# Kernel optimization log

Measured on AMD Instinct MI355X. Metric: run time of the kernel, lower is better.

Reference implementation:

```python
import jax, jax.numpy as jnp
import numpy as np

B, S, D, I, C = 4, 512, 512, 1024, 64
BASE_LR = 0.01
EPS = 1e-6


def _rms(x, w):
    return x * jax.lax.rsqrt(jnp.mean(x * x, axis=-1, keepdims=True) + EPS) * w


def _mem_apply(p, x):
    # 2-layer MLP memory: x + RMSNorm(W1 @ silu(W0 @ x))
    h = jax.nn.silu(x @ p["w0"].T)
    y = h @ p["w1"].T
    return x + _rms(y, p["ln"])


def _mem_loss(p, inp, tgt, w):
    # ((target - pred)^2 * theta).mean(-1).sum() over batch; w is scalar theta_t
    pred = _mem_apply(p, inp)
    return jnp.sum(jnp.mean((tgt - pred) ** 2 * w, axis=-1))


def _neural_memory(x, wq, wk, wv, q_norm_w, k_norm_w, alpha_w, alpha_b,
                   theta_w, theta_b, eta_w, eta_b, m_w0, m_w1, m_ln):
    b, s, d = x.shape
    nC = s // C
    params0 = {"w0": m_w0, "w1": m_w1, "ln": m_ln}
    surpr0 = jax.tree_util.tree_map(jnp.zeros_like, params0)
    xs = x.reshape(b, nC, C, d).transpose(1, 0, 2, 3)  # [nC, B, C, D]

    # per-token grads: vmap over sequence dim 1, shared params (in_dims=None)
    grad_fn = jax.vmap(jax.grad(_mem_loss), in_axes=(None, 1, 1, 0))
    idx = jnp.arange(C)

    def step(carry, xc):
        params, surpr = carry
        # adaptive gates: Linear -> sum over batch -> sigmoid (shapes [C])
        al = jax.nn.sigmoid(jnp.sum(xc @ alpha_w.T + alpha_b, axis=0))[:, 0]
        th = jax.nn.sigmoid(jnp.sum(xc @ theta_w.T + theta_b, axis=0))[:, 0] * BASE_LR
        et = jax.nn.sigmoid(jnp.sum(xc @ eta_w.T + eta_b, axis=0))[:, 0]
        k = _rms(jax.nn.silu(xc @ wk.T), k_norm_w)  # [B, C, D]
        v = jax.nn.silu(xc @ wv.T)
        grads = grad_fn(params, k, v, th)  # each leaf [C, *param_shape]
        # eta decay matrix E[m,n] = prod_{i=n+1}^m eta_i for n<=m, else 0
        M0 = jnp.where(idx[:, None] > idx[None, :], et[:, None], 1.0)
        Emat = jnp.where(idx[None, :] <= idx[:, None], jnp.cumprod(M0, axis=0), 0.0)
        c_eta = jnp.cumprod(et)  # prod_{0..m} eta
        beta = 1.0 - al
        bc_last = jnp.cumprod(beta)[-1]
        bt = jnp.cumprod(beta[::-1])[::-1]  # bt[m] = prod_{m..C-1} beta
        w_beta = jnp.concatenate([bt[1:], jnp.ones((1,), et.dtype)])

        def upd(pS, pM, u):
            # S_t = eta_t * S_{t-1} - u_t ; M_t = beta_t * M_{t-1} + S_t (vectorized)
            ex = (slice(None),) + (None,) * pS.ndim
            S_all = c_eta[ex] * pS - jnp.einsum("mn,n...->m...", Emat, u)
            newM = pM * bc_last + jnp.einsum("m,m...->...", w_beta, S_all)
            return newM, S_all[-1]

        res = {n: upd(surpr[n], params[n], grads[n]) for n in params}
        new_params = {n: res[n][0] for n in params}
        new_surpr = {n: res[n][1] for n in params}
        return (new_params, new_surpr), None

    (paramsF, _surprF), _ = jax.lax.scan(step, (params0, surpr0), xs)
    # retrieve from updated memory
    q = _rms(jax.nn.silu(x @ wq.T), q_norm_w)
    return _mem_apply(paramsF, q)


def setup_inputs() -> dict:
    key = jax.random.key(0)
    ks = jax.random.split(key, 12)

    def xavier(k, shape):
        lim = float(np.sqrt(6.0 / (shape[0] + shape[1])))
        return jax.random.uniform(k, shape, jnp.float32, -lim, lim)

    return {
        "x": jax.random.normal(ks[0], (B, S, D), jnp.float32),
        "wq": xavier(ks[1], (D, D)),
        "wk": xavier(ks[2], (D, D)),
        "wv": xavier(ks[3], (D, D)),
        "q_norm_w": jnp.ones((D,), jnp.float32),
        "k_norm_w": jnp.ones((D,), jnp.float32),
        "alpha_w": xavier(ks[4], (1, D)),
        "alpha_b": jnp.zeros((1,), jnp.float32),
        "theta_w": xavier(ks[5], (1, D)),
        "theta_b": jnp.zeros((1,), jnp.float32),
        "eta_w": xavier(ks[6], (1, D)),
        "eta_b": jnp.zeros((1,), jnp.float32),
        "m_w0": xavier(ks[7], (I, D)),
        "m_w1": xavier(ks[8], (D, I)),
        "m_ln": jnp.ones((D,), jnp.float32),
    }


def reference(x, wq, wk, wv, q_norm_w, k_norm_w, alpha_w, alpha_b,
              theta_w, theta_b, eta_w, eta_b, m_w0, m_w1, m_ln):
    return _neural_memory(x, wq, wk, wv, q_norm_w, k_norm_w, alpha_w, alpha_b,
                          theta_w, theta_b, eta_w, eta_b, m_w0, m_w1, m_ln)
```

## Files before the change

kernel.cpp:

```cpp
#include <hip/hip_runtime.h>
#include <math.h>

#define EPS 1e-6f

namespace {

typedef unsigned short u16;
typedef unsigned int u32;
typedef __bf16 bf16x8 __attribute__((ext_vector_type(8)));
typedef float f32x4 __attribute__((ext_vector_type(4)));
typedef u16 u16x8 __attribute__((ext_vector_type(8)));

constexpr int Bb = 4, Ss = 512, Dd = 512, Ii = 1024, Cc = 64;
constexpr int nCk = 8, RowsC = 256, RowsAll = 2048;

__device__ __forceinline__ float sigmoidf_(float x) { return 1.f / (1.f + expf(-x)); }
__device__ __forceinline__ float siluf_(float x)    { return x / (1.f + expf(-x)); }

__device__ __forceinline__ u16 f2bf(float f) {
  u32 u = __float_as_uint(f);
  u32 r = u + 0x7fffu + ((u >> 16) & 1u);
  return (u16)(r >> 16);
}
__device__ __forceinline__ float bf2f(u16 u) {
  return __uint_as_float(((u32)u) << 16);
}

__device__ __forceinline__ void llds16(const u16* g, u16* l) {
  __builtin_amdgcn_global_load_lds((__attribute__((address_space(1))) void*)g,
                                   (__attribute__((address_space(3))) void*)l,
                                   16, 0, 0);
}

__device__ __forceinline__ void drain_barrier() {
  asm volatile("s_waitcnt vmcnt(0)" ::: "memory");
  __builtin_amdgcn_s_barrier();
}

__device__ __forceinline__ float wave_sum(float v) {
  #pragma unroll
  for (int m = 32; m > 0; m >>= 1) v += __shfl_xor(v, m, 64);
  return v;
}

__device__ __forceinline__ float block_reduce_sum(float v, float* red) {
  int tid = threadIdx.x;
  red[tid] = v; __syncthreads();
  for (int s = 128; s > 0; s >>= 1) {
    if (tid < s) red[tid] += red[tid + s];
    __syncthreads();
  }
  float r = red[0]; __syncthreads();
  return r;
}

struct WS {
  float *w0c, *Sw0, *w1c, *Sw1, *lnc, *Sln, *tmpK, *Krows, *Vrows,
        *Yp, *gyr, *alv, *thv, *etv, *wBv, *wEv, *scal, *Qb, *Yr;
  u16 *xcb, *wkvqb, *w0b, *w1b, *w1tb, *Kb, *KT, *Ht, *dZb,
      *dYb, *dYtW, *dYtE, *dHtW, *dHtE, *Qbb, *Hrb;
};
__host__ __device__ inline WS mkws(char* base) {
  WS s; char* p = base + 256;
#define CF(nm, n) s.nm = (float*)p; p += (size_t)(n) * 4;
#define CU(nm, n) s.nm = (u16*)p;   p += (size_t)(n) * 2;
  CF(w0c, Ii*Dd) CF(Sw0, Ii*Dd) CF(w1c, Dd*Ii) CF(Sw1, Dd*Ii)
  CF(lnc, Dd) CF(Sln, Dd)
  CF(tmpK, (size_t)RowsAll*Dd) CF(Krows, (size_t)RowsAll*Dd) CF(Vrows, (size_t)RowsAll*Dd)
  CF(Yp, (size_t)16*RowsC*Dd) CF(gyr, RowsC*Dd)
  CF(alv, Ss) CF(thv, Ss) CF(etv, Ss) CF(wBv, nCk*RowsC) CF(wEv, nCk*RowsC) CF(scal, nCk*4)
  CF(Qb, (size_t)RowsAll*Dd) CF(Yr, (size_t)RowsAll*Dd)
  CU(xcb, (size_t)RowsAll*Dd) CU(wkvqb, (size_t)3*Dd*Dd)
  CU(w0b, (size_t)Ii*Dd) CU(w1b, (size_t)2*Dd*Ii) CU(w1tb, (size_t)2*Ii*Dd)
  CU(Kb, (size_t)RowsAll*Dd) CU(KT, (size_t)RowsAll*Dd)
  CU(Ht, RowsC*Ii) CU(dZb, RowsC*Ii)
  CU(dYb, RowsC*Dd) CU(dYtW, RowsC*Dd) CU(dYtE, RowsC*Dd)
  CU(dHtW, RowsC*Ii) CU(dHtE, RowsC*Ii)
  CU(Qbb, (size_t)RowsAll*Dd) CU(Hrb, (size_t)RowsAll*Ii)
#undef CF
#undef CU
  return s;
}

template<int BK, int NBUF, int EPI>
__device__ void tile64(
    u16* smA, u16* smB,
    const u16* __restrict__ A, const u16* __restrict__ Bt,
    int K, int N, int bm, int bn,
    float* C0, float* C1, float* C2,
    u16* CbT, u16* CbT2,
    const u16* Zb, const float* wB, const float* wE, int trM)
{
  constexpr int CPR = BK / 8;
  constexpr int NISS = (64 * CPR) / 256;
  constexpr int BUF = 64 * BK;
  const int tid = threadIdx.x;
  const int l = tid & 63, lr = l & 15, lq = l >> 4;
  const int w = tid >> 6, wr = w >> 1, wc = w & 1;

  f32x4 acc[2][2];
  #pragma unroll
  for (int i = 0; i < 2; ++i)
    #pragma unroll
    for (int j = 0; j < 2; ++j) acc[i][j] = f32x4{0.f, 0.f, 0.f, 0.f};

  auto stage = [&](int k0, int buf) {
    u16* dA = smA + buf * BUF;
    u16* dB = smB + buf * BUF;
    #pragma unroll
    for (int i = 0; i < NISS; ++i) {
      int e = i * 256 + tid;
      int r = e / CPR, c = (e & (CPR - 1)) ^ (r & (CPR - 1));
      llds16(A  + (size_t)(bm + r) * K + k0 + c * 8, dA + e * 8);
      llds16(Bt + (size_t)(bn + r) * K + k0 + c * 8, dB + e * 8);
    }
  };

  stage(0, 0);
  drain_barrier();
  const int nt = K / BK;
  int cur = 0;
  for (int t = 0; t < nt; ++t) {
    if (t + 1 < nt) stage((t + 1) * BK, (cur ^ 1) & (NBUF - 1));
    const u16* sA = smA + cur * BUF;
    const u16* sB = smB + cur * BUF;
    #pragma unroll
    for (int kk = 0; kk < BK / 32; ++kk) {
      bf16x8 av[2], bv[2];
      #pragma unroll
      for (int m = 0; m < 2; ++m) {
        int r = wr * 32 + m * 16 + lr;
        int c = (kk * 4 + lq) ^ (r & (CPR - 1));
        av[m] = *reinterpret_cast<const bf16x8*>(&sA[r * BK + c * 8]);
      }
      #pragma unroll
      for (int n = 0; n < 2; ++n) {
        int r = wc * 32 + n * 16 + lr;
        int c = (kk * 4 + lq) ^ (r & (CPR - 1));
        bv[n] = *reinterpret_cast<const bf16x8*>(&sB[r * BK + c * 8]);
      }
      #pragma unroll
      for (int m = 0; m < 2; ++m)
        #pragma unroll
        for (int n = 0; n < 2; ++n)
          acc[m][n] = __builtin_amdgcn_mfma_f32_16x16x32_bf16(av[m], bv[n], acc[m][n], 0, 0, 0);
    }
    drain_barrier();
    cur = (cur ^ 1) & (NBUF - 1);
  }

  #pragma unroll
  for (int m = 0; m < 2; ++m) {
    int gr0 = bm + wr * 32 + m * 16 + lq * 4;
    float wbq[4], weq[4];
    if (EPI == 3) {
      #pragma unroll
      for (int q = 0; q < 4; ++q) { wbq[q] = wB[gr0 + q]; weq[q] = wE[gr0 + q]; }
    }
    #pragma unroll
    for (int n = 0; n < 2; ++n) {
      int gc = bn + wc * 32 + n * 16 + lr;
      ushort4 t1, t2;
      #pragma unroll
      for (int q = 0; q < 4; ++q) {
        float v = acc[m][n][q];
        size_t idx = (size_t)(gr0 + q) * N + gc;
        if (EPI == 0) {
          C0[idx] = v;
        } else if (EPI == 1) {
          size_t rb = (size_t)(gr0 + q) * Dd;
          if (gc < Dd)            C0[rb + gc] = v;
          else if (gc < 2 * Dd)   C1[rb + gc - Dd] = siluf_(v);
          else                    C2[rb + gc - 2 * Dd] = v;
        } else if (EPI == 3) {
          float dh = v * bf2f(Zb[idx]);
          ((u16*)&t1)[q] = f2bf(dh * wbq[q]);
          ((u16*)&t2)[q] = f2bf(dh * weq[q]);
        }
      }
      if (EPI == 3) {
        *reinterpret_cast<ushort4*>(&CbT[(size_t)gc * trM + gr0]) = t1;
        *reinterpret_cast<ushort4*>(&CbT2[(size_t)gc * trM + gr0]) = t2;
      }
    }
  }
}

template<int BK, int NBUF, bool TR>
__device__ void gtile64(
    u16* smA, u16* smB, u16* smE,
    const u16* __restrict__ AW, const u16* __restrict__ AE,
    const u16* __restrict__ Bt,
    float* P, float* Sm, u16* Pb, u16* PbT, const float* scal,
    int M, int N, int K, int bm, int bn)
{
  constexpr int CPR = BK / 8;
  constexpr int NISS = (64 * CPR) / 256;
  constexpr int BUF = 64 * BK;
  const int tid = threadIdx.x;
  const int l = tid & 63, lr = l & 15, lq = l >> 4;
  const int w = tid >> 6, wr = w >> 1, wc = w & 1;

  f32x4 aM[2][2], aE[2][2];
  #pragma unroll
  for (int i = 0; i < 2; ++i)
    #pragma unroll
    for (int j = 0; j < 2; ++j) {
      aM[i][j] = f32x4{0.f, 0.f, 0.f, 0.f};
      aE[i][j] = f32x4{0.f, 0.f, 0.f, 0.f};
    }

  auto stage = [&](int k0, int buf) {
    u16* dA = smA + buf * BUF;
    u16* dE = smE + buf * BUF;
    u16* dB = smB + buf * BUF;
    #pragma unroll
    for (int i = 0; i < NISS; ++i) {
      int e = i * 256 + tid;
      int r = e / CPR, c = (e & (CPR - 1)) ^ (r & (CPR - 1));
      llds16(AW + (size_t)(bm + r) * K + k0 + c * 8, dA + e * 8);
      llds16(AE + (size_t)(bm + r) * K + k0 + c * 8, dE + e * 8);
      llds16(Bt + (size_t)(bn + r) * K + k0 + c * 8, dB + e * 8);
    }
  };

  stage(0, 0);
  drain_barrier();
  const int nt = K / BK;
  int cur = 0;
  for (int t = 0; t < nt; ++t) {
    if (t + 1 < nt) stage((t + 1) * BK, (cur ^ 1) & (NBUF - 1));
    const u16* sA = smA + cur * BUF;
    const u16* sE = smE + cur * BUF;
    const u16* sB = smB + cur * BUF;
    #pragma unroll
    for (int kk = 0; kk < BK / 32; ++kk) {
      bf16x8 awv[2], aev[2], bv[2];
      #pragma unroll
      for (int m = 0; m < 2; ++m) {
        int r = wr * 32 + m * 16 + lr;
        int c = (kk * 4 + lq) ^ (r & (CPR - 1));
        awv[m] = *reinterpret_cast<const bf16x8*>(&sA[r * BK + c * 8]);
        aev[m] = *reinterpret_cast<const bf16x8*>(&sE[r * BK + c * 8]);
      }
      #pragma unroll
      for (int n = 0; n < 2; ++n) {
        int r = wc * 32 + n * 16 + lr;
        int c = (kk * 4 + lq) ^ (r & (CPR - 1));
        bv[n] = *reinterpret_cast<const bf16x8*>(&sB[r * BK + c * 8]);
      }
      #pragma unroll
      for (int m = 0; m < 2; ++m)
        #pragma unroll
        for (int n = 0; n < 2; ++n) {
          aM[m][n] = __builtin_amdgcn_mfma_f32_16x16x32_bf16(awv[m], bv[n], aM[m][n], 0, 0, 0);
          aE[m][n] = __builtin_amdgcn_mfma_f32_16x16x32_bf16(aev[m], bv[n], aE[m][n], 0, 0, 0);
        }
    }
    drain_barrier();
    cur = (cur ^ 1) & (NBUF - 1);
  }

  float s0 = scal[0], s1 = scal[1], s2 = scal[2];
  #pragma unroll
  for (int m = 0; m < 2; ++m) {
    int gr0 = bm + wr * 32 + m * 16 + lq * 4;
    #pragma unroll
    for (int n = 0; n < 2; ++n) {
      int gc = bn + wc * 32 + n * 16 + lr;
      ushort4 t1;
      #pragma unroll
      for (int q = 0; q < 4; ++q) {
        size_t idx = (size_t)(gr0 + q) * N + gc;
        float p = P[idx], s = Sm[idx];
        float np = s0 * p + s1 * s - aM[m][n][q];
        float ns = s2 * s - aE[m][n][q];
        P[idx] = np; Sm[idx] = ns;
        Pb[idx] = f2bf(np);
        if (TR) ((u16*)&t1)[q] = f2bf(np);
      }
      if (TR) *reinterpret_cast<ushort4*>(&PbT[(size_t)gc * M + gr0]) = t1;
    }
  }
}


__global__ __launch_bounds__(256) void z0y_k(
    const u16* __restrict__ Kbc, const u16* __restrict__ w0b,
    const u16* __restrict__ w1b,
    u16* __restrict__ Ht, u16* __restrict__ dZb, float* __restrict__ Yp)
{
  __shared__ __align__(16) u16 sm[4 * 64 * 128 + 64 * 64];
  u16* Hs = sm + 4 * 64 * 128;
  const int tid = threadIdx.x;
  const int l = tid & 63, lr = l & 15, lq = l >> 4;
  const int w = tid >> 6, wr = w >> 1, wc = w & 1;
  const int tj = blockIdx.x, tr = blockIdx.y;
  const int bm = tr * 64, bn = tj * 64;

  {
    constexpr int BK = 128, CPR = 16, NISS = 4, BUF = 64 * BK;
    u16* smA = sm; u16* smB = sm + 2 * BUF;
    f32x4 acc[2][2];
    #pragma unroll
    for (int i = 0; i < 2; ++i)
      #pragma unroll
      for (int j = 0; j < 2; ++j) acc[i][j] = f32x4{0.f, 0.f, 0.f, 0.f};

    auto stage = [&](int k0, int buf) {
      u16* dA = smA + buf * BUF;
      u16* dB = smB + buf * BUF;
      #pragma unroll
      for (int i = 0; i < NISS; ++i) {
        int e = i * 256 + tid;
        int r = e / CPR, c = (e & (CPR - 1)) ^ (r & (CPR - 1));
        llds16(Kbc + (size_t)(bm + r) * Dd + k0 + c * 8, dA + e * 8);
        llds16(w0b + (size_t)(bn + r) * Dd + k0 + c * 8, dB + e * 8);
      }
    };
    stage(0, 0);
    drain_barrier();
    int cur = 0;
    for (int t = 0; t < 4; ++t) {
      if (t + 1 < 4) stage((t + 1) * BK, cur ^ 1);
      const u16* sA = smA + cur * BUF;
      const u16* sB = smB + cur * BUF;
      #pragma unroll
      for (int kk = 0; kk < 4; ++kk) {
        bf16x8 av[2], bv[2];
        #pragma unroll
        for (int m = 0; m < 2; ++m) {
          int r = wr * 32 + m * 16 + lr;
          int c = (kk * 4 + lq) ^ (r & (CPR - 1));
          av[m] = *reinterpret_cast<const bf16x8*>(&sA[r * BK + c * 8]);
        }
        #pragma unroll
        for (int n = 0; n < 2; ++n) {
          int r = wc * 32 + n * 16 + lr;
          int c = (kk * 4 + lq) ^ (r & (CPR - 1));
          bv[n] = *reinterpret_cast<const bf16x8*>(&sB[r * BK + c * 8]);
        }
        #pragma unroll
        for (int m = 0; m < 2; ++m)
          #pragma unroll
          for (int n = 0; n < 2; ++n)
            acc[m][n] = __builtin_amdgcn_mfma_f32_16x16x32_bf16(av[m], bv[n], acc[m][n], 0, 0, 0);
      }
      drain_barrier();
      cur ^= 1;
    }

    #pragma unroll
    for (int i = 0; i < 16; ++i) {
      int e = i * 256 + tid;
      int r = e >> 3, c = (e & 7) ^ (r & 7);
      llds16(w1b + (size_t)r * Ii + bn + c * 8, sm + e * 8);
    }

    #pragma unroll
    for (int m = 0; m < 2; ++m) {
      int gr0 = bm + wr * 32 + m * 16 + lq * 4;
      int rl0 = wr * 32 + m * 16 + lq * 4;
      #pragma unroll
      for (int n = 0; n < 2; ++n) {
        int gc = bn + wc * 32 + n * 16 + lr;
        int cl = wc * 32 + n * 16 + lr;
        ushort4 t1;
        #pragma unroll
        for (int q = 0; q < 4; ++q) {
          float v = acc[m][n][q];
          float sg = 1.f / (1.f + expf(-v));
          float h = v * sg;
          float ds = sg * (1.f + v * (1.f - sg));
          u16 hb = f2bf(h);
          ((u16*)&t1)[q] = hb;
          dZb[(size_t)(gr0 + q) * Ii + gc] = f2bf(ds);
          int rl = rl0 + q;
          Hs[rl * 64 + ((((cl >> 3) ^ (rl & 7)) << 3) | (cl & 7))] = hb;
        }
        *reinterpret_cast<ushort4*>(&Ht[(size_t)gc * RowsC + gr0]) = t1;
      }
    }
  }

  asm volatile("s_waitcnt vmcnt(0)" ::: "memory");
  __syncthreads();

  {
    f32x4 yacc[2][16];
    #pragma unroll
    for (int m = 0; m < 2; ++m)
      #pragma unroll
      for (int n = 0; n < 16; ++n) yacc[m][n] = f32x4{0.f, 0.f, 0.f, 0.f};

    #pragma unroll
    for (int kk = 0; kk < 2; ++kk) {
      bf16x8 av[2];
      #pragma unroll
      for (int m = 0; m < 2; ++m) {
        int r = wr * 32 + m * 16 + lr;
        int c = (kk * 4 + lq) ^ (r & 7);
        av[m] = *reinterpret_cast<const bf16x8*>(&Hs[r * 64 + c * 8]);
      }
      #pragma unroll
      for (int n = 0; n < 16; ++n) {
        int r = wc * 256 + n * 16 + lr;
        int c = (kk * 4 + lq) ^ (r & 7);
        bf16x8 bv = *reinterpret_cast<const bf16x8*>(&sm[r * 64 + c * 8]);
        #pragma unroll
        for (int m = 0; m < 2; ++m)
          yacc[m][n] = __builtin_amdgcn_mfma_f32_16x16x32_bf16(av[m], bv, yacc[m][n], 0, 0, 0);
      }
    }

    float* Yo = Yp + (size_t)tj * RowsC * Dd;
    #pragma unroll
    for (int m = 0; m < 2; ++m) {
      int gr0 = bm + wr * 32 + m * 16 + lq * 4;
      #pragma unroll
      for (int n = 0; n < 16; ++n) {
        int gc = wc * 256 + n * 16 + lr;
        #pragma unroll
        for (int q = 0; q < 4; ++q)
          Yo[(size_t)(gr0 + q) * Dd + gc] = yacc[m][n][q];
      }
    }
  }
}

__global__ __launch_bounds__(256) void s4_k(
    const u16* __restrict__ dYb, const u16* __restrict__ w1t_cur,
    const u16* __restrict__ dZb, u16* dHtW, u16* dHtE,
    const float* __restrict__ gyr, float* lnc, float* Sln,
    const u16* __restrict__ dYtW, const u16* __restrict__ dYtE,
    const u16* __restrict__ Ht,
    float* w1c, float* Sw1, u16* w1b_new, u16* w1t_new,
    const float* wB, const float* wE, const float* scal)
{
  __shared__ __align__(16) u16 sm[6 * 64 * 128];
  int j = blockIdx.x;
  if (j < 64) {
    int tm = j & 3, tn = j >> 2;
    tile64<128, 2, 3>(sm, sm + 2 * 64 * 128, dYb, w1t_cur, Dd, Ii,
                      tm * 64, tn * 64,
                      nullptr, nullptr, nullptr, dHtW, dHtE,
                      dZb, wB, wE, RowsC);
  } else if (j < 66) {
    int d = (j - 64) * 256 + threadIdx.x;
    float sm2 = 0.f, se2 = 0.f;
    for (int r = 0; r < RowsC; ++r) {
      float vv = gyr[(size_t)r * Dd + d];
      sm2 += wB[r] * vv; se2 += wE[r] * vv;
    }
    float pp = lnc[d], sn = Sln[d];
    lnc[d] = scal[0] * pp + scal[1] * sn - sm2;
    Sln[d] = scal[2] * sn - se2;
  } else {
    int q = j - 66;
    gtile64<128, 2, true>(sm, sm + 2 * 64 * 128, sm + 4 * 64 * 128,
                          dYtW, dYtE, Ht, w1c, Sw1, w1b_new, w1t_new,
                          scal, Dd, Ii, RowsC, (q >> 4) * 64, (q & 15) * 64);
  }
}

__global__ __launch_bounds__(256) void g2b_k(
    const u16* __restrict__ dHtW, const u16* __restrict__ dHtE,
    const u16* __restrict__ KTc,
    float* w0c, float* Sw0, u16* w0b, const float* scal)
{
  __shared__ __align__(16) u16 sm[6 * 64 * 128];
  int j = blockIdx.x;
  gtile64<128, 2, false>(sm, sm + 2 * 64 * 128, sm + 4 * 64 * 128,
                         dHtW, dHtE, KTc, w0c, Sw0, w0b, nullptr,
                         scal, Ii, Dd, RowsC, (j >> 3) * 64, (j & 7) * 64);
}

__global__ __launch_bounds__(256) void kvq_k(
    const u16* __restrict__ xcb, const u16* __restrict__ wkvqb,
    float* tmpK, float* Vrows, float* Yq, char* ws)
{
  __shared__ __align__(16) u16 sm[4 * 64 * 128];
  int j = blockIdx.x;
  if (j < 768) {
    int tn = j % 24, tm = j / 24;
    tile64<128, 2, 1>(sm, sm + 2 * 64 * 128, xcb, wkvqb, Dd, 3 * Dd,
                      tm * 64, tn * 64,
                      tmpK, Vrows, Yq, nullptr, nullptr,
                      nullptr, nullptr, nullptr, 0);
    return;
  }
  if (threadIdx.x != 0) return;
  WS S = mkws(ws);
  int ci = j - 768;
  const float* alc = S.alv + ci * Cc;
  const float* etc_ = S.etv + ci * Cc;
  float beta[Cc], wb[Cc], ce[Cc], E[Cc], T[Cc];
  for (int i = 0; i < Cc; ++i) beta[i] = 1.f - alc[i];
  wb[Cc - 1] = 1.f;
  for (int m = Cc - 2; m >= 0; --m) wb[m] = wb[m + 1] * beta[m + 1];
  float bc_last = wb[0] * beta[0];
  float p = 1.f, A = 0.f;
  for (int m = 0; m < Cc; ++m) { p *= etc_[m]; ce[m] = p; A += wb[m] * ce[m]; }
  E[Cc - 1] = 1.f; T[Cc - 1] = 1.f;
  for (int n = Cc - 2; n >= 0; --n) {
    E[n] = E[n + 1] * etc_[n + 1];
    T[n] = wb[n] + etc_[n + 1] * T[n + 1];
  }
  for (int b = 0; b < Bb; ++b)
    for (int t = 0; t < Cc; ++t) {
      S.wBv[ci * RowsC + b * Cc + t] = T[t];
      S.wEv[ci * RowsC + b * Cc + t] = E[t];
    }
  S.scal[ci * 4 + 0] = bc_last; S.scal[ci * 4 + 1] = A; S.scal[ci * 4 + 2] = ce[Cc - 1];
}

template<int EPI>
__global__ __launch_bounds__(256) void mgemm128_k(
    const u16* __restrict__ A, const u16* __restrict__ Bt,
    float* C0, u16* Cb, int M, int N, int K)
{
  constexpr int TS = 128, BK = 64;
  constexpr int BUF = TS * BK;
  __shared__ __align__(16) u16 As[2 * BUF];
  __shared__ __align__(16) u16 Bs[2 * BUF];
  const int tid = threadIdx.x;
  const int l = tid & 63, lr = l & 15, lq = l >> 4;
  const int w = tid >> 6, wr = w >> 1, wc = w & 1;
  const int bm = blockIdx.y * TS, bn = blockIdx.x * TS;

  f32x4 acc[4][4];
  #pragma unroll
  for (int i = 0; i < 4; ++i)
    #pragma unroll
    for (int j = 0; j < 4; ++j) acc[i][j] = f32x4{0.f, 0.f, 0.f, 0.f};

  auto stage = [&](int k0, int buf) {
    u16* dA = As + buf * BUF;
    u16* dB = Bs + buf * BUF;
    #pragma unroll
    for (int i = 0; i < 4; ++i) {
      int e = i * 256 + tid;
      int r = e >> 3, c = (e & 7) ^ (r & 7);
      llds16(A  + (size_t)(bm + r) * K + k0 + c * 8, dA + e * 8);
      llds16(Bt + (size_t)(bn + r) * K + k0 + c * 8, dB + e * 8);
    }
  };

  stage(0, 0);
  drain_barrier();
  const int nt = K / BK;
  int cur = 0;
  for (int t = 0; t < nt; ++t) {
    if (t + 1 < nt) stage((t + 1) * BK, cur ^ 1);
    const u16* sA = As + cur * BUF;
    const u16* sB = Bs + cur * BUF;
    #pragma unroll
    for (int kk = 0; kk < 2; ++kk) {
      bf16x8 av[4], bv[4];
      #pragma unroll
      for (int m = 0; m < 4; ++m) {
        int r = wr * 64 + m * 16 + lr;
        int c = (kk * 4 + lq) ^ (r & 7);
        av[m] = *reinterpret_cast<const bf16x8*>(&sA[r * BK + c * 8]);
      }
      #pragma unroll
      for (int n = 0; n < 4; ++n) {
        int r = wc * 64 + n * 16 + lr;
        int c = (kk * 4 + lq) ^ (r & 7);
        bv[n] = *reinterpret_cast<const bf16x8*>(&sB[r * BK + c * 8]);
      }
      #pragma unroll
      for (int m = 0; m < 4; ++m)
        #pragma unroll
        for (int n = 0; n < 4; ++n)
          acc[m][n] = __builtin_amdgcn_mfma_f32_16x16x32_bf16(av[m], bv[n], acc[m][n], 0, 0, 0);
    }
    drain_barrier();
    cur ^= 1;
  }

  #pragma unroll
  for (int m = 0; m < 4; ++m) {
    int gr0 = bm + wr * 64 + m * 16 + lq * 4;
    #pragma unroll
    for (int n = 0; n < 4; ++n) {
      int gc = bn + wc * 64 + n * 16 + lr;
      #pragma unroll
      for (int q = 0; q < 4; ++q) {
        size_t idx = (size_t)(gr0 + q) * N + gc;
        float v = acc[m][n][q];
        if (EPI == 0) C0[idx] = v;
        else          Cb[idx] = f2bf(siluf_(v));
      }
    }
  }
}

__global__ __launch_bounds__(256) void init_k(
    const float* __restrict__ x,
    const float* __restrict__ aw, const float* __restrict__ ab,
    const float* __restrict__ tw, const float* __restrict__ tb,
    const float* __restrict__ ew, const float* __restrict__ eb,
    const float* __restrict__ wq, const float* __restrict__ wkw,
    const float* __restrict__ wvw, const float* __restrict__ mw0,
    const float* __restrict__ mw1, const float* __restrict__ mln,
    char* ws)
{
  WS S = mkws(ws);
  const int tid = threadIdx.x;
  if (blockIdx.x < 512) {
    __shared__ float red[256];
    int s = blockIdx.x;
    int ci = s >> 6, t = s & 63;
    float sa = 0.f, st = 0.f, se = 0.f;
    for (int b = 0; b < Bb; ++b) {
      const float* xr = x + ((size_t)b * Ss + s) * Dd;
      u16* dst = S.xcb + ((size_t)(ci * RowsC + b * Cc + t)) * Dd;
      for (int d = tid; d < Dd; d += 256) {
        float v = xr[d];
        dst[d] = f2bf(v);
        sa += v * aw[d]; st += v * tw[d]; se += v * ew[d];
      }
    }
    sa = block_reduce_sum(sa, red);
    st = block_reduce_sum(st, red);
    se = block_reduce_sum(se, red);
    if (tid == 0) {
      S.alv[s] = sigmoidf_(sa + Bb * ab[0]);
      S.thv[s] = sigmoidf_(st + Bb * tb[0]) * 0.01f;
      S.etv[s] = sigmoidf_(se + Bb * eb[0]);
    }
    return;
  }
  if (blockIdx.x < 640) {
    __shared__ float t[64][65];
    int tt = blockIdx.x - 512;
    int br = (tt & 7) * 64, bc = (tt >> 3) * 64;
    #pragma unroll
    for (int i = 0; i < 16; ++i) {
      int e = tid + i * 256;
      int r = e >> 6, c = e & 63;
      t[r][c] = mw1[(size_t)(br + r) * Ii + bc + c];
    }
    __syncthreads();
    #pragma unroll
    for (int i = 0; i < 16; ++i) {
      int e = tid + i * 256;
      int rr = e >> 6, cc = e & 63;
      S.w1tb[(size_t)(bc + rr) * Dd + br + cc] = f2bf(t[cc][rr]);
    }
    return;
  }
  const int i0 = (blockIdx.x - 640) * 256 + tid;
  const int stride = 512 * 256;
  for (int i = i0; i < (Dd * Dd) / 4; i += stride) {
    float4 v = ((const float4*)wkw)[i];
    ushort4 o; o.x = f2bf(v.x); o.y = f2bf(v.y); o.z = f2bf(v.z); o.w = f2bf(v.w);
    ((ushort4*)S.wkvqb)[i] = o;
    v = ((const float4*)wvw)[i];
    o.x = f2bf(v.x); o.y = f2bf(v.y); o.z = f2bf(v.z); o.w = f2bf(v.w);
    ((ushort4*)S.wkvqb)[i + (Dd * Dd) / 4] = o;
    v = ((const float4*)wq)[i];
    o.x = f2bf(v.x); o.y = f2bf(v.y); o.z = f2bf(v.z); o.w = f2bf(v.w);
    ((ushort4*)S.wkvqb)[i + (Dd * Dd) / 2] = o;
  }
  for (int i = i0; i < (Ii * Dd) / 4; i += stride) {
    float4 z4; z4.x = z4.y = z4.z = z4.w = 0.f;
    float4 v = ((const float4*)mw0)[i];
    ((float4*)S.w0c)[i] = v; ((float4*)S.Sw0)[i] = z4;
    ushort4 o; o.x = f2bf(v.x); o.y = f2bf(v.y); o.z = f2bf(v.z); o.w = f2bf(v.w);
    ((ushort4*)S.w0b)[i] = o;
    v = ((const float4*)mw1)[i];
    ((float4*)S.w1c)[i] = v; ((float4*)S.Sw1)[i] = z4;
    o.x = f2bf(v.x); o.y = f2bf(v.y); o.z = f2bf(v.z); o.w = f2bf(v.w);
    ((ushort4*)S.w1b)[i] = o;
  }
  for (int i = i0; i < Dd; i += stride) { S.lnc[i] = mln[i]; S.Sln[i] = 0.f; }
}

__global__ __launch_bounds__(256) void norm2_k(
    const float* __restrict__ tmpK, const float* __restrict__ Yq,
    float* Krows, u16* Kb, u16* KT,
    float* Qb, u16* Qbb,
    const float* __restrict__ kn, const float* __restrict__ qn)
{
  __shared__ u16 lt[4][Dd];
  const int tid = threadIdx.x, w = tid >> 6, l = tid & 63;
  const bool isQ = blockIdx.x >= 512;
  const int r0 = (isQ ? (int)blockIdx.x - 512 : (int)blockIdx.x) * 4;
  const int row = r0 + w, d0 = l * 8;
  const float* in = (isQ ? Yq : tmpK) + (size_t)row * Dd + d0;
  const float* nw = (isQ ? qn : kn) + d0;
  float v[8];
  *(float4*)&v[0] = *(const float4*)in;
  *(float4*)&v[4] = *(const float4*)(in + 4);
  float ss = 0.f;
  #pragma unroll
  for (int j = 0; j < 8; ++j) { v[j] = siluf_(v[j]); ss += v[j] * v[j]; }
  ss = wave_sum(ss);
  float rr = rsqrtf(ss / (float)Dd + EPS);
  float nv[8];
  *(float4*)&nv[0] = *(const float4*)nw;
  *(float4*)&nv[4] = *(const float4*)(nw + 4);
  float y[8]; u16x8 pb;
  #pragma unroll
  for (int j = 0; j < 8; ++j) { y[j] = v[j] * rr * nv[j]; pb[j] = f2bf(y[j]); }
  float* outf = (isQ ? Qb : Krows) + (size_t)row * Dd + d0;
  u16* outb = (isQ ? Qbb : Kb) + (size_t)row * Dd + d0;
  *(float4*)outf       = *(float4*)&y[0];
  *(float4*)(outf + 4) = *(float4*)&y[4];
  *(u16x8*)outb = pb;
  if (!isQ) {
    int ci = r0 >> 8, rloc = r0 & 255;
    u16* KTc = KT + (size_t)ci * Dd * RowsC;
    #pragma unroll
    for (int j = 0; j < 8; ++j) lt[w][d0 + j] = pb[j];
    __syncthreads();
    for (int d = tid; d < Dd; d += 256) {
      ushort4 pk;
      pk.x = lt[0][d]; pk.y = lt[1][d]; pk.z = lt[2][d]; pk.w = lt[3][d];
      *reinterpret_cast<ushort4*>(&KTc[(size_t)d * RowsC + rloc]) = pk;
    }
  }
}

__global__ __launch_bounds__(256) void loss_back4_k(
    const float* __restrict__ Kr, const float* __restrict__ Vr,
    const float* __restrict__ Yp, const float* __restrict__ lnc,
    const float* __restrict__ th, const float* __restrict__ wB,
    const float* __restrict__ wE,
    u16* __restrict__ dYb, u16* __restrict__ dYtW, u16* __restrict__ dYtE,
    float* __restrict__ gyr)
{
  __shared__ u16 lw[4][Dd];
  __shared__ u16 le[4][Dd];
  const int tid = threadIdx.x, w = tid >> 6, l = tid & 63;
  const int row = blockIdx.x * 4 + w, t = row & 63, d0 = l * 8;
  size_t base = (size_t)row * Dd + d0;

  float y[8] = {0.f, 0.f, 0.f, 0.f, 0.f, 0.f, 0.f, 0.f};
  #pragma unroll
  for (int p2 = 0; p2 < 16; ++p2) {
    const float* yp = Yp + (size_t)p2 * (RowsC * Dd) + base;
    float4 u0 = *(const float4*)yp;
    float4 u1 = *(const float4*)(yp + 4);
    y[0] += u0.x; y[1] += u0.y; y[2] += u0.z; y[3] += u0.w;
    y[4] += u1.x; y[5] += u1.y; y[6] += u1.z; y[7] += u1.w;
  }

  float kk[8], vv[8], lv[8];
  *(float4*)&kk[0] = *(const float4*)(Kr + base);
  *(float4*)&kk[4] = *(const float4*)(Kr + base + 4);
  *(float4*)&vv[0] = *(const float4*)(Vr + base);
  *(float4*)&vv[4] = *(const float4*)(Vr + base + 4);
  *(float4*)&lv[0] = *(const float4*)(lnc + d0);
  *(float4*)&lv[4] = *(const float4*)(lnc + d0 + 4);

  float ss = 0.f;
  #pragma unroll
  for (int q = 0; q < 8; ++q) ss += y[q] * y[q];
  ss = wave_sum(ss);
  float rr = rsqrtf(ss / (float)Dd + EPS);
  float c = 2.f * th[t] / (float)Dd;

  float g[8], s2 = 0.f;
  #pragma unroll
  for (int q = 0; q < 8; ++q) {
    g[q] = c * ((kk[q] + y[q] * rr * lv[q]) - vv[q]);
    s2 += g[q] * lv[q] * y[q];
  }
  s2 = wave_sum(s2);
  float coef = rr * rr * rr * s2 / (float)Dd;

  float wb = wB[row], we = wE[row];
  u16x8 pb; float gy[8];
  #pragma unroll
  for (int q = 0; q < 8; ++q) {
    float dv = rr * g[q] * lv[q] - coef * y[q];
    pb[q] = f2bf(dv);
    lw[w][d0 + q] = f2bf(dv * wb);
    le[w][d0 + q] = f2bf(dv * we);
    gy[q] = g[q] * y[q] * rr;
  }
  *(u16x8*)(dYb + base) = pb;
  *(float4*)(gyr + base)     = *(float4*)&gy[0];
  *(float4*)(gyr + base + 4) = *(float4*)&gy[4];

  __syncthreads();
  int r0 = blockIdx.x * 4;
  for (int d = tid; d < Dd; d += 256) {
    ushort4 pw, pe;
    pw.x = lw[0][d]; pw.y = lw[1][d]; pw.z = lw[2][d]; pw.w = lw[3][d];
    pe.x = le[0][d]; pe.y = le[1][d]; pe.z = le[2][d]; pe.w = le[3][d];
    *reinterpret_cast<ushort4*>(&dYtW[(size_t)d * RowsC + r0]) = pw;
    *reinterpret_cast<ushort4*>(&dYtE[(size_t)d * RowsC + r0]) = pe;
  }
}

__global__ __launch_bounds__(256) void final4_k(
    const float* __restrict__ Q, const float* __restrict__ Y,
    const float* __restrict__ lnc, float* __restrict__ out)
{
  const int tid = threadIdx.x, w = tid >> 6, l = tid & 63;
  const int row = blockIdx.x * 4 + w;
  const int ci = row >> 8, wi = row & 255, b = wi >> 6, t = wi & 63;
  const int d0 = l * 8;
  const float* yr = Y + (size_t)row * Dd + d0;
  float y[8];
  *(float4*)&y[0] = *(const float4*)yr;
  *(float4*)&y[4] = *(const float4*)(yr + 4);
  float ss = 0.f;
  #pragma unroll
  for (int q = 0; q < 8; ++q) ss += y[q] * y[q];
  ss = wave_sum(ss);
  float rr = rsqrtf(ss / (float)Dd + EPS);
  const float* qb = Q + (size_t)row * Dd + d0;
  const float* lf = lnc + d0;
  float o[8];
  #pragma unroll
  for (int q = 0; q < 8; ++q) o[q] = qb[q] + y[q] * rr * lf[q];
  float* ob = out + ((size_t)b * Ss + ci * Cc + t) * Dd + d0;
  *(float4*)ob       = *(float4*)&o[0];
  *(float4*)(ob + 4) = *(float4*)&o[4];
}

}

extern "C" void kernel_launch(void* const* d_in, const int* in_sizes, int n_in,
                              void* d_out, int out_size, void* d_ws, size_t ws_size,
                              hipStream_t stream)
{
  const float* x   = (const float*)d_in[0];
  const float* wq  = (const float*)d_in[1];
  const float* wkw = (const float*)d_in[2];
  const float* wvw = (const float*)d_in[3];
  const float* qn  = (const float*)d_in[4];
  const float* kn  = (const float*)d_in[5];
  const float* aw  = (const float*)d_in[6];
  const float* ab  = (const float*)d_in[7];
  const float* tw  = (const float*)d_in[8];
  const float* tb  = (const float*)d_in[9];
  const float* ew  = (const float*)d_in[10];
  const float* eb  = (const float*)d_in[11];
  const float* mw0 = (const float*)d_in[12];
  const float* mw1 = (const float*)d_in[13];
  const float* mln = (const float*)d_in[14];
  float* out = (float*)d_out;
  char* ws = (char*)d_ws;
  WS S = mkws(ws);

  init_k<<<1152, 256, 0, stream>>>(x, aw, ab, tw, tb, ew, eb,
                                   wq, wkw, wvw, mw0, mw1, mln, ws);
  kvq_k<<<776, 256, 0, stream>>>(S.xcb, S.wkvqb, S.tmpK, S.Vrows, S.Yr, ws);
  norm2_k<<<1024, 256, 0, stream>>>(S.tmpK, S.Yr, S.Krows, S.Kb, S.KT,
                                    S.Qb, S.Qbb, kn, qn);

  for (int ci = 0; ci < nCk; ++ci) {
    const int p = ci & 1;
    const u16* Kbc = S.Kb + (size_t)ci * RowsC * Dd;
    const u16* KTc = S.KT + (size_t)ci * Dd * RowsC;
    const float* Krc = S.Krows + (size_t)ci * RowsC * Dd;
    const float* Vrc = S.Vrows + (size_t)ci * RowsC * Dd;
    const float* scc = S.scal + ci * 4;
    const float* wBc = S.wBv + ci * RowsC;
    const float* wEc = S.wEv + ci * RowsC;
    const float* thc = S.thv + ci * Cc;
    u16* w1b_cur = S.w1b + (size_t)p * Dd * Ii;
    u16* w1b_new = S.w1b + (size_t)(p ^ 1) * Dd * Ii;
    u16* w1t_cur = S.w1tb + (size_t)p * Ii * Dd;
    u16* w1t_new = S.w1tb + (size_t)(p ^ 1) * Ii * Dd;

    z0y_k<<<dim3(16, 4), 256, 0, stream>>>(
        Kbc, S.w0b, w1b_cur, S.Ht, S.dZb, S.Yp);
    loss_back4_k<<<RowsC / 4, 256, 0, stream>>>(
        Krc, Vrc, S.Yp, S.lnc, thc, wBc, wEc, S.dYb, S.dYtW, S.dYtE, S.gyr);
    s4_k<<<194, 256, 0, stream>>>(
        S.dYb, w1t_cur, S.dZb, S.dHtW, S.dHtE, S.gyr, S.lnc, S.Sln,
        S.dYtW, S.dYtE, S.Ht, S.w1c, S.Sw1, w1b_new, w1t_new,
        wBc, wEc, scc);
    g2b_k<<<128, 256, 0, stream>>>(
        S.dHtW, S.dHtE, KTc, S.w0c, S.Sw0, S.w0b, scc);
  }

  mgemm128_k<4><<<dim3(Ii / 128, RowsAll / 128), 256, 0, stream>>>(
      S.Qbb, S.w0b, nullptr, S.Hrb, RowsAll, Ii, Dd);
  mgemm128_k<0><<<dim3(Dd / 128, RowsAll / 128), 256, 0, stream>>>(
      S.Hrb, S.w1b, S.Yr, nullptr, RowsAll, Dd, Ii);
  final4_k<<<RowsAll / 4, 256, 0, stream>>>(S.Qb, S.Yr, S.lnc, out);
}
```

Baseline: 385.6 us.

## Fuse row RMSNorm epilogues into full-row GEMMs for K/Q projections and output

```diff
diff --git a/kernel.cpp b/kernel.cpp
--- a/kernel.cpp
+++ b/kernel.cpp
@@ -55,8 +55,8 @@
 }
 
 struct WS {
-  float *w0c, *Sw0, *w1c, *Sw1, *lnc, *Sln, *tmpK, *Krows, *Vrows,
-        *Yp, *gyr, *alv, *thv, *etv, *wBv, *wEv, *scal, *Qb, *Yr;
+  float *w0c, *Sw0, *w1c, *Sw1, *lnc, *Sln, *Krows, *Vrows,
+        *Yp, *gyr, *alv, *thv, *etv, *wBv, *wEv, *scal, *Qb;
   u16 *xcb, *wkvqb, *w0b, *w1b, *w1tb, *Kb, *KT, *Ht, *dZb,
       *dYb, *dYtW, *dYtE, *dHtW, *dHtE, *Qbb, *Hrb;
 };
@@ -66,10 +66,10 @@
 #define CU(nm, n) s.nm = (u16*)p;   p += (size_t)(n) * 2;
   CF(w0c, Ii*Dd) CF(Sw0, Ii*Dd) CF(w1c, Dd*Ii) CF(Sw1, Dd*Ii)
   CF(lnc, Dd) CF(Sln, Dd)
-  CF(tmpK, (size_t)RowsAll*Dd) CF(Krows, (size_t)RowsAll*Dd) CF(Vrows, (size_t)RowsAll*Dd)
+  CF(Krows, (size_t)RowsAll*Dd) CF(Vrows, (size_t)RowsAll*Dd)
   CF(Yp, (size_t)16*RowsC*Dd) CF(gyr, RowsC*Dd)
   CF(alv, Ss) CF(thv, Ss) CF(etv, Ss) CF(wBv, nCk*RowsC) CF(wEv, nCk*RowsC) CF(scal, nCk*4)
-  CF(Qb, (size_t)RowsAll*Dd) CF(Yr, (size_t)RowsAll*Dd)
+  CF(Qb, (size_t)RowsAll*Dd)
   CU(xcb, (size_t)RowsAll*Dd) CU(wkvqb, (size_t)3*Dd*Dd)
   CU(w0b, (size_t)Ii*Dd) CU(w1b, (size_t)2*Dd*Ii) CU(w1tb, (size_t)2*Ii*Dd)
   CU(Kb, (size_t)RowsAll*Dd) CU(KT, (size_t)RowsAll*Dd)
@@ -87,8 +87,7 @@
     u16* smA, u16* smB,
     const u16* __restrict__ A, const u16* __restrict__ Bt,
     int K, int N, int bm, int bn,
-    float* C0, float* C1, float* C2,
-    u16* CbT, u16* CbT2,
+    float* C0, u16* CbT, u16* CbT2,
     const u16* Zb, const float* wB, const float* wE, int trM)
 {
   constexpr int CPR = BK / 8;
@@ -167,15 +166,12 @@
         size_t idx = (size_t)(gr0 + q) * N + gc;
         if (EPI == 0) {
           C0[idx] = v;
-        } else if (EPI == 1) {
-          size_t rb = (size_t)(gr0 + q) * Dd;
-          if (gc < Dd)            C0[rb + gc] = v;
-          else if (gc < 2 * Dd)   C1[rb + gc - Dd] = siluf_(v);
-          else                    C2[rb + gc - 2 * Dd] = v;
         } else if (EPI == 3) {
           float dh = v * bf2f(Zb[idx]);
           ((u16*)&t1)[q] = f2bf(dh * wbq[q]);
           ((u16*)&t2)[q] = f2bf(dh * weq[q]);
+        } else if (EPI == 5) {
+          C0[idx] = siluf_(v);
         }
       }
       if (EPI == 3) {
@@ -280,6 +276,134 @@
         if (TR) ((u16*)&t1)[q] = f2bf(np);
       }
       if (TR) *reinterpret_cast<ushort4*>(&PbT[(size_t)gc * M + gr0]) = t1;
+    }
+  }
+}
+
+template<int KTOT, int EPI>
+__device__ void rowgemm(u16* sm,
+    const u16* __restrict__ A, const u16* __restrict__ Bt, int bm,
+    float* C0f, u16* C0b, u16* KT, const float* nw,
+    const float* Qb2, float* out)
+{
+  constexpr int BK = 32, CPR = 4;
+  constexpr int ABUF = 64 * BK, BBUF = 512 * BK;
+  u16* smA = sm;
+  u16* smB = sm + 2 * ABUF;
+  const int tid = threadIdx.x;
+  const int l = tid & 63, lr = l & 15, lq = l >> 4;
+  const int w = tid >> 6;
+
+  f32x4 acc[32];
+  #pragma unroll
+  for (int n = 0; n < 32; ++n) acc[n] = f32x4{0.f, 0.f, 0.f, 0.f};
+
+  auto stage = [&](int k0, int buf) {
+    {
+      int e = tid;
+      int r = e >> 2, c = (e & 3) ^ (r & 3);
+      llds16(A + (size_t)(bm + r) * KTOT + k0 + c * 8, smA + buf * ABUF + e * 8);
+    }
+    #pragma unroll
+    for (int i = 0; i < 8; ++i) {
+      int e = i * 256 + tid;
+      int r = e >> 2, c = (e & 3) ^ (r & 3);
+      llds16(Bt + (size_t)r * KTOT + k0 + c * 8, smB + buf * BBUF + e * 8);
+    }
+  };
+
+  stage(0, 0);
+  drain_barrier();
+  const int nt = KTOT / BK;
+  int cur = 0;
+  for (int t = 0; t < nt; ++t) {
+    if (t + 1 < nt) stage((t + 1) * BK, cur ^ 1);
+    const u16* sA = smA + cur * ABUF;
+    const u16* sB = smB + cur * BBUF;
+    int ra = w * 16 + lr;
+    int ca = lq ^ (ra & 3);
+    bf16x8 av = *reinterpret_cast<const bf16x8*>(&sA[ra * BK + ca * 8]);
+    #pragma unroll
+    for (int n = 0; n < 32; ++n) {
+      int rb = n * 16 + lr;
+      int cb = lq ^ (rb & 3);
+      bf16x8 bv = *reinterpret_cast<const bf16x8*>(&sB[rb * BK + cb * 8]);
+      acc[n] = __builtin_amdgcn_mfma_f32_16x16x32_bf16(av, bv, acc[n], 0, 0, 0);
+    }
+    drain_barrier();
+    cur ^= 1;
+  }
+
+  if (EPI == 0 || EPI == 1) {
+    float ssq[4] = {0.f, 0.f, 0.f, 0.f};
+    #pragma unroll
+    for (int n = 0; n < 32; ++n)
+      #pragma unroll
+      for (int q = 0; q < 4; ++q) {
+        float s = siluf_(acc[n][q]);
+        acc[n][q] = s;
+        ssq[q] += s * s;
+      }
+    #pragma unroll
+    for (int q = 0; q < 4; ++q) {
+      #pragma unroll
+      for (int msk = 1; msk < 16; msk <<= 1) ssq[q] += __shfl_xor(ssq[q], msk, 64);
+      ssq[q] = rsqrtf(ssq[q] / (float)Dd + EPS);
+    }
+    const int rl0 = w * 16 + lq * 4;
+    u16* lt = sm;
+    #pragma unroll
+    for (int n = 0; n < 32; ++n) {
+      int col = n * 16 + lr;
+      float nv = nw[col];
+      #pragma unroll
+      for (int q = 0; q < 4; ++q) {
+        float y = acc[n][q] * ssq[q] * nv;
+        u16 yb = f2bf(y);
+        size_t idx = (size_t)(bm + rl0 + q) * Dd + col;
+        C0f[idx] = y;
+        C0b[idx] = yb;
+        if (EPI == 0) lt[(rl0 + q) * 516 + col] = yb;
+      }
+    }
+    if (EPI == 0) {
+      __syncthreads();
+      int ci = bm >> 8, rloc = bm & 255;
+      u16* KTc = KT + (size_t)ci * Dd * RowsC;
+      #pragma unroll
+      for (int i = 0; i < 16; ++i) {
+        int task = i * 256 + tid;
+        int col = task >> 3, g = task & 7;
+        u16x8 pk;
+        #pragma unroll
+        for (int j = 0; j < 8; ++j) pk[j] = lt[(g * 8 + j) * 516 + col];
+        *reinterpret_cast<u16x8*>(&KTc[(size_t)col * RowsC + rloc + g * 8]) = pk;
+      }
+    }
+  } else {
+    float ssq[4] = {0.f, 0.f, 0.f, 0.f};
+    #pragma unroll
+    for (int n = 0; n < 32; ++n)
+      #pragma unroll
+      for (int q = 0; q < 4; ++q) ssq[q] += acc[n][q] * acc[n][q];
+    #pragma unroll
+    for (int q = 0; q < 4; ++q) {
+      #pragma unroll
+      for (int msk = 1; msk < 16; msk <<= 1) ssq[q] += __shfl_xor(ssq[q], msk, 64);
+      ssq[q] = rsqrtf(ssq[q] / (float)Dd + EPS);
+    }
+    const int rl0 = w * 16 + lq * 4;
+    #pragma unroll
+    for (int q = 0; q < 4; ++q) {
+      int row = bm + rl0 + q;
+      int ci = row >> 8, wi = row & 255, b = wi >> 6, t = wi & 63;
+      float* ob = out + ((size_t)b * Ss + ci * Cc + t) * Dd;
+      const float* qb = Qb2 + (size_t)row * Dd;
+      #pragma unroll
+      for (int n = 0; n < 32; ++n) {
+        int col = n * 16 + lr;
+        ob[col] = qb[col] + acc[n][q] * ssq[q] * nw[col];
+      }
     }
   }
 }
@@ -443,8 +567,7 @@
     int tm = j & 3, tn = j >> 2;
     tile64<128, 2, 3>(sm, sm + 2 * 64 * 128, dYb, w1t_cur, Dd, Ii,
                       tm * 64, tn * 64,
-                      nullptr, nullptr, nullptr, dHtW, dHtE,
-                      dZb, wB, wE, RowsC);
+                      nullptr, dHtW, dHtE, dZb, wB, wE, RowsC);
   } else if (j < 66) {
     int d = (j - 64) * 256 + threadIdx.x;
     float sm2 = 0.f, se2 = 0.f;
@@ -477,21 +600,32 @@
 
 __global__ __launch_bounds__(256) void kvq_k(
     const u16* __restrict__ xcb, const u16* __restrict__ wkvqb,
-    float* tmpK, float* Vrows, float* Yq, char* ws)
-{
-  __shared__ __align__(16) u16 sm[4 * 64 * 128];
+    float* Krows, u16* Kb, u16* KT, float* Vrows,
+    float* Qb, u16* Qbb,
+    const float* __restrict__ kn, const float* __restrict__ qn, char* ws)
+{
+  __shared__ __align__(16) u16 sm[2 * 64 * 32 + 2 * 512 * 32];
   int j = blockIdx.x;
-  if (j < 768) {
-    int tn = j % 24, tm = j / 24;
-    tile64<128, 2, 1>(sm, sm + 2 * 64 * 128, xcb, wkvqb, Dd, 3 * Dd,
-                      tm * 64, tn * 64,
-                      tmpK, Vrows, Yq, nullptr, nullptr,
-                      nullptr, nullptr, nullptr, 0);
+  if (j < 256) {
+    int tn = j & 7, tm = j >> 3;
+    tile64<128, 2, 5>(sm, sm + 2 * 64 * 128, xcb, wkvqb + (size_t)Dd * Dd,
+                      Dd, Dd, tm * 64, tn * 64,
+                      Vrows, nullptr, nullptr, nullptr, nullptr, nullptr, 0);
+    return;
+  }
+  if (j < 288) {
+    rowgemm<Dd, 0>(sm, xcb, wkvqb, (j - 256) * 64,
+                   Krows, Kb, KT, kn, nullptr, nullptr);
+    return;
+  }
+  if (j < 320) {
+    rowgemm<Dd, 1>(sm, xcb, wkvqb + (size_t)2 * Dd * Dd, (j - 288) * 64,
+                   Qb, Qbb, nullptr, qn, nullptr, nullptr);
     return;
   }
   if (threadIdx.x != 0) return;
   WS S = mkws(ws);
-  int ci = j - 768;
+  int ci = j - 320;
   const float* alc = S.alv + ci * Cc;
   const float* etc_ = S.etv + ci * Cc;
   float beta[Cc], wb[Cc], ce[Cc], E[Cc], T[Cc];
@@ -514,10 +648,19 @@
   S.scal[ci * 4 + 0] = bc_last; S.scal[ci * 4 + 1] = A; S.scal[ci * 4 + 2] = ce[Cc - 1];
 }
 
-template<int EPI>
-__global__ __launch_bounds__(256) void mgemm128_k(
+__global__ __launch_bounds__(256) void yfin_k(
+    const u16* __restrict__ Hrb, const u16* __restrict__ w1b,
+    const float* __restrict__ Qb, const float* __restrict__ lnc,
+    float* __restrict__ out)
+{
+  __shared__ __align__(16) u16 sm[2 * 64 * 32 + 2 * 512 * 32];
+  rowgemm<Ii, 2>(sm, Hrb, w1b, blockIdx.x * 64,
+                 nullptr, nullptr, nullptr, lnc, Qb, out);
+}
+
+__global__ __launch_bounds__(256) void mgemm128s_k(
     const u16* __restrict__ A, const u16* __restrict__ Bt,
-    float* C0, u16* Cb, int M, int N, int K)
+    u16* Cb, int M, int N, int K)
 {
   constexpr int TS = 128, BK = 64;
   constexpr int BUF = TS * BK;
@@ -586,12 +729,8 @@
     for (int n = 0; n < 4; ++n) {
       int gc = bn + wc * 64 + n * 16 + lr;
       #pragma unroll
-      for (int q = 0; q < 4; ++q) {
-        size_t idx = (size_t)(gr0 + q) * N + gc;
-        float v = acc[m][n][q];
-        if (EPI == 0) C0[idx] = v;
-        else          Cb[idx] = f2bf(siluf_(v));
-      }
+      for (int q = 0; q < 4; ++q)
+        Cb[(size_t)(gr0 + q) * N + gc] = f2bf(siluf_(acc[m][n][q]));
     }
   }
 }
@@ -678,52 +817,6 @@
   for (int i = i0; i < Dd; i += stride) { S.lnc[i] = mln[i]; S.Sln[i] = 0.f; }
 }
 
-__global__ __launch_bounds__(256) void norm2_k(
-    const float* __restrict__ tmpK, const float* __restrict__ Yq,
-    float* Krows, u16* Kb, u16* KT,
-    float* Qb, u16* Qbb,
-    const float* __restrict__ kn, const float* __restrict__ qn)
-{
-  __shared__ u16 lt[4][Dd];
-  const int tid = threadIdx.x, w = tid >> 6, l = tid & 63;
-  const bool isQ = blockIdx.x >= 512;
-  const int r0 = (isQ ? (int)blockIdx.x - 512 : (int)blockIdx.x) * 4;
-  const int row = r0 + w, d0 = l * 8;
-  const float* in = (isQ ? Yq : tmpK) + (size_t)row * Dd + d0;
-  const float* nw = (isQ ? qn : kn) + d0;
-  float v[8];
-  *(float4*)&v[0] = *(const float4*)in;
-  *(float4*)&v[4] = *(const float4*)(in + 4);
-  float ss = 0.f;
-  #pragma unroll
-  for (int j = 0; j < 8; ++j) { v[j] = siluf_(v[j]); ss += v[j] * v[j]; }
-  ss = wave_sum(ss);
-  float rr = rsqrtf(ss / (float)Dd + EPS);
-  float nv[8];
-  *(float4*)&nv[0] = *(const float4*)nw;
-  *(float4*)&nv[4] = *(const float4*)(nw + 4);
-  float y[8]; u16x8 pb;
-  #pragma unroll
-  for (int j = 0; j < 8; ++j) { y[j] = v[j] * rr * nv[j]; pb[j] = f2bf(y[j]); }
-  float* outf = (isQ ? Qb : Krows) + (size_t)row * Dd + d0;
-  u16* outb = (isQ ? Qbb : Kb) + (size_t)row * Dd + d0;
-  *(float4*)outf       = *(float4*)&y[0];
-  *(float4*)(outf + 4) = *(float4*)&y[4];
-  *(u16x8*)outb = pb;
-  if (!isQ) {
-    int ci = r0 >> 8, rloc = r0 & 255;
-    u16* KTc = KT + (size_t)ci * Dd * RowsC;
-    #pragma unroll
-    for (int j = 0; j < 8; ++j) lt[w][d0 + j] = pb[j];
-    __syncthreads();
-    for (int d = tid; d < Dd; d += 256) {
-      ushort4 pk;
-      pk.x = lt[0][d]; pk.y = lt[1][d]; pk.z = lt[2][d]; pk.w = lt[3][d];
-      *reinterpret_cast<ushort4*>(&KTc[(size_t)d * RowsC + rloc]) = pk;
-    }
-  }
-}
-
 __global__ __launch_bounds__(256) void loss_back4_k(
     const float* __restrict__ Kr, const float* __restrict__ Vr,
     const float* __restrict__ Yp, const float* __restrict__ lnc,
@@ -795,33 +888,6 @@
     *reinterpret_cast<ushort4*>(&dYtW[(size_t)d * RowsC + r0]) = pw;
     *reinterpret_cast<ushort4*>(&dYtE[(size_t)d * RowsC + r0]) = pe;
   }
-}
-
-__global__ __launch_bounds__(256) void final4_k(
-    const float* __restrict__ Q, const float* __restrict__ Y,
-    const float* __restrict__ lnc, float* __restrict__ out)
-{
-  const int tid = threadIdx.x, w = tid >> 6, l = tid & 63;
-  const int row = blockIdx.x * 4 + w;
-  const int ci = row >> 8, wi = row & 255, b = wi >> 6, t = wi & 63;
-  const int d0 = l * 8;
-  const float* yr = Y + (size_t)row * Dd + d0;
-  float y[8];
-  *(float4*)&y[0] = *(const float4*)yr;
-  *(float4*)&y[4] = *(const float4*)(yr + 4);
-  float ss = 0.f;
-  #pragma unroll
-  for (int q = 0; q < 8; ++q) ss += y[q] * y[q];
-  ss = wave_sum(ss);
-  float rr = rsqrtf(ss / (float)Dd + EPS);
-  const float* qb = Q + (size_t)row * Dd + d0;
-  const float* lf = lnc + d0;
-  float o[8];
-  #pragma unroll
-  for (int q = 0; q < 8; ++q) o[q] = qb[q] + y[q] * rr * lf[q];
-  float* ob = out + ((size_t)b * Ss + ci * Cc + t) * Dd + d0;
-  *(float4*)ob       = *(float4*)&o[0];
-  *(float4*)(ob + 4) = *(float4*)&o[4];
 }
 
 }
@@ -851,9 +917,8 @@
 
   init_k<<<1152, 256, 0, stream>>>(x, aw, ab, tw, tb, ew, eb,
                                    wq, wkw, wvw, mw0, mw1, mln, ws);
-  kvq_k<<<776, 256, 0, stream>>>(S.xcb, S.wkvqb, S.tmpK, S.Vrows, S.Yr, ws);
-  norm2_k<<<1024, 256, 0, stream>>>(S.tmpK, S.Yr, S.Krows, S.Kb, S.KT,
-                                    S.Qb, S.Qbb, kn, qn);
+  kvq_k<<<328, 256, 0, stream>>>(S.xcb, S.wkvqb, S.Krows, S.Kb, S.KT,
+                                 S.Vrows, S.Qb, S.Qbb, kn, qn, ws);
 
   for (int ci = 0; ci < nCk; ++ci) {
     const int p = ci & 1;
@@ -882,9 +947,7 @@
         S.dHtW, S.dHtE, KTc, S.w0c, S.Sw0, S.w0b, scc);
   }
 
-  mgemm128_k<4><<<dim3(Ii / 128, RowsAll / 128), 256, 0, stream>>>(
-      S.Qbb, S.w0b, nullptr, S.Hrb, RowsAll, Ii, Dd);
-  mgemm128_k<0><<<dim3(Dd / 128, RowsAll / 128), 256, 0, stream>>>(
-      S.Hrb, S.w1b, S.Yr, nullptr, RowsAll, Dd, Ii);
-  final4_k<<<RowsAll / 4, 256, 0, stream>>>(S.Qb, S.Yr, S.lnc, out);
-}
+  mgemm128s_k<<<dim3(Ii / 128, RowsAll / 128), 256, 0, stream>>>(
+      S.Qbb, S.w0b, S.Hrb, RowsAll, Ii, Dd);
+  yfin_k<<<RowsAll / 64, 256, 0, stream>>>(S.Hrb, S.w1b, S.Qb, S.lnc, out);
+}
```

New measurement: 412.7 us. 1.07x slower.
